# Kernel optimization log

Measured on AMD Instinct MI355X. Metric: run time of the kernel, lower is better.

## Reference

```python
import jax, jax.numpy as jnp
import numpy as np

TOTAL_DIM = 64  # 16+16+16+8+8
HIDDEN = 4 * TOTAL_DIM
NUM_HEADS = 8


def _fourier(x, num_freqs):
    # Dyadic Fourier features: sin/cos of 2^j * x for j in [0, num_freqs).
    # Output dim = input_dim * num_freqs * 2 (matches embed_dim in the module).
    freqs = 2.0 ** jnp.arange(num_freqs, dtype=x.dtype)  # (F,)
    phase = x[..., :, None] * freqs                       # (..., in, F)
    out = jnp.concatenate([jnp.sin(phase), jnp.cos(phase)], axis=-1)  # (..., in, 2F)
    return out.reshape(x.shape[:-1] + (-1,))


def setup_inputs() -> dict:
    key = jax.random.key(0)
    k1, k2, k3, k4, k5, k6 = jax.random.split(key, 6)
    B, Nq, Nk, D = 8, 256, 256, 10
    query_states = jax.random.normal(k1, (B, Nq, D), dtype=jnp.float32)
    key_states = jax.random.normal(k2, (B, Nk, D), dtype=jnp.float32)
    W1 = jax.random.normal(k3, (TOTAL_DIM, HIDDEN), dtype=jnp.float32) / np.sqrt(TOTAL_DIM)
    b1 = jnp.zeros((HIDDEN,), dtype=jnp.float32)
    W2 = jax.random.normal(k4, (HIDDEN, NUM_HEADS), dtype=jnp.float32) / np.sqrt(HIDDEN)
    b2 = jnp.zeros((NUM_HEADS,), dtype=jnp.float32)
    return {"query_states": query_states, "key_states": key_states,
            "W1": W1, "b1": b1, "W2": W2, "b2": b2}


def _features(query_states, key_states):
    # Slice per-ship fields, then broadcast pairwise: q -> (B,Nq,1,*), k -> (B,1,Nk,*)
    q_team = query_states[:, :, None, 0]          # (B,Nq,1)
    k_team = key_states[:, None, :, 0]            # (B,1,Nk)
    q_pos = query_states[:, :, None, 3:5]
    k_pos = key_states[:, None, :, 3:5]
    q_vel = query_states[:, :, None, 5:7]
    k_vel = key_states[:, None, :, 5:7]
    q_att = query_states[:, :, None, 7:9]
    k_att = key_states[:, None, :, 7:9]

    delta_pos = k_pos - q_pos                     # (B,Nq,Nk,2)
    delta_vel = k_vel - q_vel                     # (B,Nq,Nk,2)
    feat_delta_input = jnp.concatenate([delta_pos, delta_vel], axis=-1)  # (B,Nq,Nk,4)

    dist_sq = jnp.sum(delta_pos ** 2, axis=-1, keepdims=True)
    dist = jnp.sqrt(dist_sq + 1e-6)
    inv_dist = 1.0 / (dist + 0.1)
    feat_dist_input = jnp.concatenate([dist, inv_dist], axis=-1)         # (B,Nq,Nk,2)

    bearing = delta_pos / (dist + 1e-6)
    ata = jnp.sum(bearing * q_att, axis=-1, keepdims=True)
    aspect = jnp.sum(bearing * k_att, axis=-1, keepdims=True)
    feat_angle_input = jnp.concatenate([ata, aspect], axis=-1)           # (B,Nq,Nk,2)

    dot_dp_dv = jnp.sum(delta_pos * delta_vel, axis=-1, keepdims=True)
    speed_sq = jnp.sum(delta_vel ** 2, axis=-1, keepdims=True)
    ttca = jnp.tanh(jax.nn.relu(-dot_dp_dv / (speed_sq + 1e-6)))
    feat_intercept_input = jnp.concatenate([ttca, dist], axis=-1)        # (B,Nq,Nk,2)

    same_team = (q_team == k_team).astype(query_states.dtype)[..., None]
    q_speed = jnp.linalg.norm(q_vel, axis=-1, keepdims=True)
    k_speed = jnp.linalg.norm(k_vel, axis=-1, keepdims=True)
    delta_speed = k_speed - q_speed
    feat_team_input = jnp.concatenate([same_team, delta_speed], axis=-1)  # (B,Nq,Nk,2)

    out_dist = _fourier(feat_dist_input, 4)        # 16
    out_angle = _fourier(feat_angle_input, 4)      # 16
    out_delta = _fourier(feat_delta_input, 2)      # 16
    out_intercept = _fourier(feat_intercept_input, 2)  # 8
    out_team = _fourier(feat_team_input, 2)        # 8
    return jnp.concatenate([out_dist, out_angle, out_delta, out_intercept, out_team], axis=-1)


def reference(query_states, key_states, W1, b1, W2, b2):
    combined = _features(query_states, key_states)          # (B,Nq,Nk,64)
    h = jax.nn.silu(combined @ W1 + b1)                     # (B,Nq,Nk,256)
    bias = h @ W2 + b2                                      # (B,Nq,Nk,H)
    return jnp.transpose(bias, (0, 3, 1, 2))                # (B,H,Nq,Nk)
```

## Files before the change

### kernel.cpp

```cpp
#include <hip/hip_runtime.h>
#include <math.h>

#define NB 8
#define NQ 256
#define NK 256
#define DIN 10
#define FDIM 64
#define HIDDEN 256
#define NH 8

#define FSTRIDE 72
#define HSTRIDE 264

typedef float f32x4 __attribute__((ext_vector_type(4)));
typedef short bf16x8 __attribute__((ext_vector_type(8)));

__device__ __forceinline__ short f2bf(float f) {
    return (short)((__float_as_uint(f) + 0x8000u) >> 16);
}
__device__ __forceinline__ unsigned pack2(float a, float b) {
    unsigned ua = __float_as_uint(a) + 0x8000u;
    unsigned ub = __float_as_uint(b) + 0x8000u;
    return __builtin_amdgcn_perm(ub, ua, 0x07060302);
}

__device__ __forceinline__ void four4(float x, float* dst) {
    float s1 = __sinf(x), c1 = __cosf(x);
    float s2 = 2.f * s1 * c1, c2 = 1.f - 2.f * s1 * s1;
    float s4 = 2.f * s2 * c2, c4 = 1.f - 2.f * s2 * s2;
    float s8 = 2.f * s4 * c4, c8 = 1.f - 2.f * s4 * s4;
    dst[0] = s1; dst[1] = s2; dst[2] = s4; dst[3] = s8;
    dst[4] = c1; dst[5] = c2; dst[6] = c4; dst[7] = c8;
}
__device__ __forceinline__ void four2(float x, float* dst) {
    float s1 = __sinf(x), c1 = __cosf(x);
    dst[0] = s1; dst[1] = 2.f * s1 * c1;
    dst[2] = c1; dst[3] = 1.f - 2.f * s1 * s1;
}

__global__ __launch_bounds__(256, 2) void relfeat_mfma_kernel(
    const float* __restrict__ q, const float* __restrict__ k,
    const float* __restrict__ W1, const float* __restrict__ b1,
    const float* __restrict__ W2, const float* __restrict__ b2,
    float* __restrict__ out)
{
    __shared__ __align__(16) short feat_s[NK * FSTRIDE];
    __shared__ __align__(16) short h_s[64 * HSTRIDE];
    __shared__ __align__(16) short w2_s[16 * HSTRIDE];

    const int t = threadIdx.x;
    const int wave = t >> 6;
    const int lane15 = t & 15;
    const int quad = (t >> 4) & 3;
    const int b = blockIdx.x >> 8;
    const int i = blockIdx.x & (NQ - 1);

    {
        const float* kp = k + ((size_t)b * NK + t) * DIN;
        const float k0 = kp[0], k3 = kp[3], k4 = kp[4], k5 = kp[5], k6 = kp[6],
                    k7 = kp[7], k8 = kp[8];
        const float* qp = q + ((size_t)b * NQ + i) * DIN;
        const float q0 = qp[0], q3 = qp[3], q4 = qp[4], q5 = qp[5], q6 = qp[6],
                    q7 = qp[7], q8 = qp[8];

        const float dpx = k3 - q3, dpy = k4 - q4;
        const float dvx = k5 - q5, dvy = k6 - q6;
        const float dist = sqrtf(dpx * dpx + dpy * dpy + 1e-6f);
        const float inv_dist = 1.0f / (dist + 0.1f);
        const float inv_d2 = 1.0f / (dist + 1e-6f);
        const float bear_x = dpx * inv_d2, bear_y = dpy * inv_d2;
        const float ata = bear_x * q7 + bear_y * q8;
        const float aspect = bear_x * k7 + bear_y * k8;
        const float dot_dp_dv = dpx * dvx + dpy * dvy;
        const float speed_sq = dvx * dvx + dvy * dvy;
        const float ttca = tanhf(fmaxf(0.f, -dot_dp_dv / (speed_sq + 1e-6f)));
        const float same_team = (q0 == k0) ? 1.f : 0.f;
        const float q_speed = sqrtf(q5 * q5 + q6 * q6);
        const float k_speed = sqrtf(k5 * k5 + k6 * k6);
        const float delta_speed = k_speed - q_speed;

        float feat[FDIM];
        four4(dist,        feat + 0);
        four4(inv_dist,    feat + 8);
        four4(ata,         feat + 16);
        four4(aspect,      feat + 24);
        four2(dpx,         feat + 32);
        four2(dpy,         feat + 36);
        four2(dvx,         feat + 40);
        four2(dvy,         feat + 44);
        four2(ttca,        feat + 48);
        four2(dist,        feat + 52);
        four2(same_team,   feat + 56);
        four2(delta_speed, feat + 60);

#pragma unroll
        for (int c8 = 0; c8 < 8; ++c8) {
            uint4 v;
            v.x = pack2(feat[c8 * 8 + 0], feat[c8 * 8 + 1]);
            v.y = pack2(feat[c8 * 8 + 2], feat[c8 * 8 + 3]);
            v.z = pack2(feat[c8 * 8 + 4], feat[c8 * 8 + 5]);
            v.w = pack2(feat[c8 * 8 + 6], feat[c8 * 8 + 7]);
            *(uint4*)&feat_s[t * FSTRIDE + c8 * 8] = v;
        }
    }

    for (int idx = t; idx < 8 * HSTRIDE; idx += 256) w2_s[8 * HSTRIDE + idx] = 0;
#pragma unroll
    for (int o = 0; o < NH; ++o) w2_s[o * HSTRIDE + t] = f2bf(W2[t * NH + o]);

    const int n0 = wave * 64;
    bf16x8 bfrag[4][2];
#pragma unroll
    for (int nt = 0; nt < 4; ++nt)
#pragma unroll
        for (int ks = 0; ks < 2; ++ks) {
            const float* wp = W1 + (size_t)(ks * 32 + quad * 8) * HIDDEN
                              + (n0 + nt * 16 + lane15);
            bf16x8 v;
#pragma unroll
            for (int e = 0; e < 8; ++e) v[e] = f2bf(wp[(size_t)e * HIDDEN]);
            bfrag[nt][ks] = v;
        }
    float b1f[4];
#pragma unroll
    for (int nt = 0; nt < 4; ++nt) b1f[nt] = b1[n0 + nt * 16 + lane15];
    const float b2v = (lane15 < NH) ? b2[lane15] : 0.f;

    __syncthreads();

#pragma unroll 1
    for (int m = 0; m < 4; ++m) {
        const int p0 = m * 64;

        f32x4 acc[4][4];
#pragma unroll
        for (int mt = 0; mt < 4; ++mt)
#pragma unroll
            for (int nt = 0; nt < 4; ++nt) {
                const float bb = b1f[nt];
                acc[mt][nt] = (f32x4){bb, bb, bb, bb};
            }
#pragma unroll
        for (int ks = 0; ks < 2; ++ks)
#pragma unroll
            for (int mt = 0; mt < 4; ++mt) {
                const bf16x8 a = *(const bf16x8*)&feat_s[(p0 + mt * 16 + lane15) * FSTRIDE
                                                          + ks * 32 + quad * 8];
#pragma unroll
                for (int nt = 0; nt < 4; ++nt)
                    acc[mt][nt] = __builtin_amdgcn_mfma_f32_16x16x32_bf16(
                        a, bfrag[nt][ks], acc[mt][nt], 0, 0, 0);
            }

#pragma unroll
        for (int mt = 0; mt < 4; ++mt)
#pragma unroll
            for (int nt = 0; nt < 4; ++nt) {
                const int h = n0 + nt * 16 + lane15;
#pragma unroll
                for (int r = 0; r < 4; ++r) {
                    const int pair = mt * 16 + quad * 4 + r;
                    const float p = acc[mt][nt][r];
                    const float e = __builtin_amdgcn_exp2f(p * -1.44269504f);
                    const float s = p * __builtin_amdgcn_rcpf(1.f + e);
                    h_s[pair * HSTRIDE + h] = f2bf(s);
                }
            }
        __syncthreads();

        const int pw = wave * 16;
        f32x4 acc2 = (f32x4){b2v, b2v, b2v, b2v};
#pragma unroll
        for (int ks = 0; ks < 8; ++ks) {
            const bf16x8 ha = *(const bf16x8*)&h_s[(pw + lane15) * HSTRIDE
                                                    + ks * 32 + quad * 8];
            const bf16x8 wb = *(const bf16x8*)&w2_s[lane15 * HSTRIDE
                                                     + ks * 32 + quad * 8];
            acc2 = __builtin_amdgcn_mfma_f32_16x16x32_bf16(ha, wb, acc2, 0, 0, 0);
        }
        if (lane15 < NH) {
            float* op = out + (((size_t)b * NH + lane15) * NQ + i) * NK
                        + (p0 + pw + quad * 4);
            *(float4*)op = make_float4(acc2[0], acc2[1], acc2[2], acc2[3]);
        }
        __syncthreads();
    }
}

extern "C" void kernel_launch(void* const* d_in, const int* in_sizes, int n_in,
                              void* d_out, int out_size, void* d_ws, size_t ws_size,
                              hipStream_t stream) {
    const float* q  = (const float*)d_in[0];
    const float* k  = (const float*)d_in[1];
    const float* W1 = (const float*)d_in[2];
    const float* b1 = (const float*)d_in[3];
    const float* W2 = (const float*)d_in[4];
    const float* b2 = (const float*)d_in[5];
    float* out = (float*)d_out;

    dim3 grid(NB * NQ);
    dim3 block(NK);
    relfeat_mfma_kernel<<<grid, block, 0, stream>>>(q, k, W1, b1, W2, b2, out);
}
```

Before: 120.2 us.

## Shrink LDS footprint with XOR-swizzled features and half-size hidden tiles for occupancy

```diff
diff --git a/kernel.cpp b/kernel.cpp
--- a/kernel.cpp
+++ b/kernel.cpp
@@ -9,8 +9,9 @@
 #define HIDDEN 256
 #define NH 8
 
-#define FSTRIDE 72
+#define FSTRIDE 64
 #define HSTRIDE 264
+#define W2S 256
 
 typedef float f32x4 __attribute__((ext_vector_type(4)));
 typedef short bf16x8 __attribute__((ext_vector_type(8)));
@@ -38,15 +39,15 @@
     dst[2] = c1; dst[3] = 1.f - 2.f * s1 * s1;
 }
 
-__global__ __launch_bounds__(256, 2) void relfeat_mfma_kernel(
+__global__ __launch_bounds__(256, 3) void relfeat_mfma_kernel(
     const float* __restrict__ q, const float* __restrict__ k,
     const float* __restrict__ W1, const float* __restrict__ b1,
     const float* __restrict__ W2, const float* __restrict__ b2,
     float* __restrict__ out)
 {
     __shared__ __align__(16) short feat_s[NK * FSTRIDE];
-    __shared__ __align__(16) short h_s[64 * HSTRIDE];
-    __shared__ __align__(16) short w2_s[16 * HSTRIDE];
+    __shared__ __align__(16) short h_s[32 * HSTRIDE];
+    __shared__ __align__(16) short w2_s[8 * W2S];
 
     const int t = threadIdx.x;
     const int wave = t >> 6;
@@ -93,6 +94,7 @@
         four2(same_team,   feat + 56);
         four2(delta_speed, feat + 60);
 
+        const int sw = t & 7;
 #pragma unroll
         for (int c8 = 0; c8 < 8; ++c8) {
             uint4 v;
@@ -100,13 +102,12 @@
             v.y = pack2(feat[c8 * 8 + 2], feat[c8 * 8 + 3]);
             v.z = pack2(feat[c8 * 8 + 4], feat[c8 * 8 + 5]);
             v.w = pack2(feat[c8 * 8 + 6], feat[c8 * 8 + 7]);
-            *(uint4*)&feat_s[t * FSTRIDE + c8 * 8] = v;
+            *(uint4*)&feat_s[t * FSTRIDE + ((c8 ^ sw) * 8)] = v;
         }
     }
 
-    for (int idx = t; idx < 8 * HSTRIDE; idx += 256) w2_s[8 * HSTRIDE + idx] = 0;
-#pragma unroll
-    for (int o = 0; o < NH; ++o) w2_s[o * HSTRIDE + t] = f2bf(W2[t * NH + o]);
+#pragma unroll
+    for (int o = 0; o < NH; ++o) w2_s[o * W2S + t] = f2bf(W2[t * NH + o]);
 
     const int n0 = wave * 64;
     bf16x8 bfrag[4][2];
@@ -128,13 +129,14 @@
 
     __syncthreads();
 
+    const int swr = lane15 & 7;
 #pragma unroll 1
-    for (int m = 0; m < 4; ++m) {
-        const int p0 = m * 64;
-
-        f32x4 acc[4][4];
-#pragma unroll
-        for (int mt = 0; mt < 4; ++mt)
+    for (int hc = 0; hc < 8; ++hc) {
+        const int p0h = hc * 32;
+
+        f32x4 acc[2][4];
+#pragma unroll
+        for (int mt = 0; mt < 2; ++mt)
 #pragma unroll
             for (int nt = 0; nt < 4; ++nt) {
                 const float bb = b1f[nt];
@@ -143,9 +145,10 @@
 #pragma unroll
         for (int ks = 0; ks < 2; ++ks)
 #pragma unroll
-            for (int mt = 0; mt < 4; ++mt) {
-                const bf16x8 a = *(const bf16x8*)&feat_s[(p0 + mt * 16 + lane15) * FSTRIDE
-                                                          + ks * 32 + quad * 8];
+            for (int mt = 0; mt < 2; ++mt) {
+                const int row = p0h + mt * 16 + lane15;
+                const bf16x8 a = *(const bf16x8*)
+                    &feat_s[row * FSTRIDE + (((ks * 4 + quad) ^ swr) * 8)];
 #pragma unroll
                 for (int nt = 0; nt < 4; ++nt)
                     acc[mt][nt] = __builtin_amdgcn_mfma_f32_16x16x32_bf16(
@@ -153,35 +156,37 @@
             }
 
 #pragma unroll
-        for (int mt = 0; mt < 4; ++mt)
+        for (int mt = 0; mt < 2; ++mt)
 #pragma unroll
             for (int nt = 0; nt < 4; ++nt) {
                 const int h = n0 + nt * 16 + lane15;
 #pragma unroll
                 for (int r = 0; r < 4; ++r) {
                     const int pair = mt * 16 + quad * 4 + r;
-                    const float p = acc[mt][nt][r];
-                    const float e = __builtin_amdgcn_exp2f(p * -1.44269504f);
-                    const float s = p * __builtin_amdgcn_rcpf(1.f + e);
+                    const float pv = acc[mt][nt][r];
+                    const float e = __builtin_amdgcn_exp2f(pv * -1.44269504f);
+                    const float s = pv * __builtin_amdgcn_rcpf(1.f + e);
                     h_s[pair * HSTRIDE + h] = f2bf(s);
                 }
             }
         __syncthreads();
 
-        const int pw = wave * 16;
-        f32x4 acc2 = (f32x4){b2v, b2v, b2v, b2v};
-#pragma unroll
-        for (int ks = 0; ks < 8; ++ks) {
-            const bf16x8 ha = *(const bf16x8*)&h_s[(pw + lane15) * HSTRIDE
-                                                    + ks * 32 + quad * 8];
-            const bf16x8 wb = *(const bf16x8*)&w2_s[lane15 * HSTRIDE
-                                                     + ks * 32 + quad * 8];
-            acc2 = __builtin_amdgcn_mfma_f32_16x16x32_bf16(ha, wb, acc2, 0, 0, 0);
-        }
-        if (lane15 < NH) {
-            float* op = out + (((size_t)b * NH + lane15) * NQ + i) * NK
-                        + (p0 + pw + quad * 4);
-            *(float4*)op = make_float4(acc2[0], acc2[1], acc2[2], acc2[3]);
+        if (wave < 2) {
+            const int pw = wave * 16;
+            f32x4 acc2 = (f32x4){b2v, b2v, b2v, b2v};
+#pragma unroll
+            for (int ks = 0; ks < 8; ++ks) {
+                const bf16x8 ha = *(const bf16x8*)&h_s[(pw + lane15) * HSTRIDE
+                                                        + ks * 32 + quad * 8];
+                const bf16x8 wb = *(const bf16x8*)&w2_s[(lane15 & 7) * W2S
+                                                         + ks * 32 + quad * 8];
+                acc2 = __builtin_amdgcn_mfma_f32_16x16x32_bf16(ha, wb, acc2, 0, 0, 0);
+            }
+            if (lane15 < NH) {
+                float* op = out + (((size_t)b * NH + lane15) * NQ + i) * NK
+                            + (p0h + pw + quad * 4);
+                *(float4*)op = make_float4(acc2[0], acc2[1], acc2[2], acc2[3]);
+            }
         }
         __syncthreads();
     }
```

Measured after the change: 117.8 us. 1.02x faster.
